# Optimization experiments

Measured on AMD Instinct MI355X. Metric: run time of the kernel, lower is better.

The kernel has to match this reference:

```python
import jax, jax.numpy as jnp
import numpy as np

NUM_HEADS = 4
WINDOW = 3

def setup_inputs() -> dict:
    key = jax.random.key(0)
    ks = jax.random.split(key, 6)
    B, V, C, H, W = 4, 6, 256, 32, 32
    s = 0.02
    return {
        "x": jax.random.normal(ks[0], (B, V, C, H, W), jnp.float32),
        "Wq": jax.random.normal(ks[1], (C, C), jnp.float32) * s,
        "bq": jnp.zeros((C,), jnp.float32),
        "Wk": jax.random.normal(ks[2], (V * C, C), jnp.float32) * s,
        "bk": jnp.zeros((C,), jnp.float32),
        "Wv": jax.random.normal(ks[3], (V * C, C), jnp.float32) * s,
        "bv": jnp.zeros((C,), jnp.float32),
        "Wo": jax.random.normal(ks[4], (C, C), jnp.float32) * s,
        "bo": jnp.zeros((C,), jnp.float32),
    }

def reference(x, Wq, bq, Wk, bk, Wv, bv, Wo, bo):
    B, V, C, H, W = x.shape
    HW = H * W
    S = HW * V  # query sequence length
    nh = NUM_HEADS
    hd = C // nh
    # q: [B, V, H, W, C] -> [B, S, C]
    q_in = jnp.transpose(x, (0, 1, 3, 4, 2)).reshape(B, S, C)
    # k/v input: [B, H, W, V, C] -> [B, HW, V*C]
    kv_in = jnp.transpose(x, (0, 3, 4, 1, 2)).reshape(B, HW, V * C)
    q = q_in @ Wq + bq
    k = kv_in @ Wk + bk
    v = kv_in @ Wv + bv
    q = q.reshape(B, S, nh, hd).transpose(0, 2, 1, 3)    # [B, nh, S, hd]
    k = k.reshape(B, HW, nh, hd).transpose(0, 2, 1, 3)   # [B, nh, HW, hd]
    v = v.reshape(B, HW, nh, hd).transpose(0, 2, 1, 3)   # [B, nh, HW, hd]
    logits = jnp.einsum("bhqd,bhkd->bhqk", q, k) / jnp.sqrt(jnp.float32(hd))
    # Faithful mask: row i has ones in columns [max(0,i-W), i+W] (clipped to HW cols);
    # it is ADDED as mask * -1e9, masking OUT the diagonal window (as in source).
    i = jnp.arange(S)[:, None]
    j = jnp.arange(HW)[None, :]
    mask = ((j >= i - WINDOW) & (j < i + WINDOW + 1)).astype(logits.dtype)
    logits = logits + mask * (-1e9)
    attn = jax.nn.softmax(logits, axis=-1)
    out = jnp.einsum("bhqk,bhkd->bhqd", attn, v)         # [B, nh, S, hd]
    out = out.transpose(0, 2, 1, 3).reshape(B, S, C)
    out = out @ Wo + bo
    return x.reshape(B * V, C, H, W) + out.reshape(B * V, C, H, W)
```

## Files before the change

### kernel.cpp

```cpp
#include <hip/hip_runtime.h>
#include <cstddef>

namespace {

constexpr int B=4, V=6, C=256, HWS=1024, S=6144, NH=4, HD=64, VC=1536;

typedef short short8  __attribute__((ext_vector_type(8)));
typedef short short4v __attribute__((ext_vector_type(4)));
typedef float f32x4   __attribute__((ext_vector_type(4)));

__device__ inline short f2bf(float f){
  union{float f; unsigned u;} v; v.f=f;
  unsigned r = v.u + 0x7fffu + ((v.u>>16)&1u);
  return (short)(r>>16);
}
__device__ inline unsigned fbits(float f){
  union{float f; unsigned u;} v; v.f=f; return v.u;
}

__device__ inline void tr_tile(const float* in, int inRow, short* out, int outRow,
                               int r0, int c0, short* T , int t){
  {
    const int rr=t>>2, cc=(t&3)*16;
    const float* p = in + (size_t)(r0+rr)*inRow + c0 + cc;
    short tmp[16];
    #pragma unroll
    for(int j=0;j<4;j++){
      const float4 f=*(const float4*)(p+j*4);
      tmp[j*4+0]=f2bf(f.x); tmp[j*4+1]=f2bf(f.y);
      tmp[j*4+2]=f2bf(f.z); tmp[j*4+3]=f2bf(f.w);
    }
    *(short8*)&T[rr*72+cc]   = *(short8*)&tmp[0];
    *(short8*)&T[rr*72+cc+8] = *(short8*)&tmp[8];
  }
  __syncthreads();
  {
    const int cc=t>>2, rr0=(t&3)*16;
    short tmp[16];
    #pragma unroll
    for(int j=0;j<16;j++) tmp[j]=T[(rr0+j)*72+cc];
    short* o = out + (size_t)(c0+cc)*outRow + r0 + rr0;
    *(short8*)o     = *(short8*)&tmp[0];
    *(short8*)(o+8) = *(short8*)&tmp[8];
  }
}

__global__ __launch_bounds__(256) void prep(const float* __restrict__ x,
                                            const float* __restrict__ Wq, const float* __restrict__ Wk,
                                            const float* __restrict__ Wv, const float* __restrict__ Wo,
                                            short* __restrict__ xb, short* __restrict__ WqT,
                                            short* __restrict__ WkT, short* __restrict__ WvT,
                                            short* __restrict__ WoT){
  __shared__ short T[64*72];
  const int blk=blockIdx.x;
  if(blk<1536){
    const int bx=blk&15, by=(blk>>4)&3, bv=blk>>6;
    tr_tile(x + (size_t)bv*C*HWS, HWS, xb + (size_t)bv*HWS*C, C, by*64, bx*64, T, threadIdx.x);
  } else {
    const int idx=blk-1536;
    const int tile=idx%96, z=idx/96;
    const float* in; short* out; int R;
    if(z==0){in=Wq; out=WqT; R=C;}
    else if(z==1){in=Wo; out=WoT; R=C;}
    else if(z==2){in=Wk; out=WkT; R=VC;}
    else         {in=Wv; out=WvT; R=VC;}
    const int tilesC=C/64, ntiles=(R/64)*tilesC;
    if(tile>=ntiles) return;
    tr_tile(in, C, out, R, (tile/tilesC)*64, (tile%tilesC)*64, T, threadIdx.x);
  }
}

template<int MODE>
__device__ inline void qo_body(const short* __restrict__ A, const short* __restrict__ BT,
                               const float* __restrict__ bias, const float* __restrict__ xres,
                               void* __restrict__ outv, short* As, short* Bs, int n0, int r0){
  const int t=threadIdx.x, lane=t&63, w=t>>6, quad=lane>>4, ln=lane&15;
  f32x4 acc[2][4];
  #pragma unroll
  for(int rt=0;rt<2;rt++)
    #pragma unroll
    for(int nt=0;nt<4;nt++) acc[rt][nt]=(f32x4)0.f;

  for(int k0=0;k0<C;k0+=64){
    if(k0) __syncthreads();
    { const int r=t>>1, c=(t&1)*32;
      const short* p = A + (size_t)(r0+r)*C + k0 + c;
      #pragma unroll
      for(int j=0;j<4;j++) *(short8*)&As[r*72+c+j*8] = *(const short8*)(p+j*8);
    }
    { const int n=t>>2, c=(t&3)*16;
      const short* p = BT + (size_t)(n0+n)*C + k0 + c;
      *(short8*)&Bs[n*72+c]   = *(const short8*)p;
      *(short8*)&Bs[n*72+c+8] = *(const short8*)(p+8);
    }
    __syncthreads();
    #pragma unroll
    for(int s=0;s<2;s++){
      short8 af0=*(short8*)&As[(w*32+ln)*72    + s*32+quad*8];
      short8 af1=*(short8*)&As[(w*32+16+ln)*72 + s*32+quad*8];
      #pragma unroll
      for(int nt=0;nt<4;nt++){
        const short8 bf=*(short8*)&Bs[(nt*16+ln)*72 + s*32+quad*8];
        acc[0][nt]=__builtin_amdgcn_mfma_f32_16x16x32_bf16(af0,bf,acc[0][nt],0,0,0);
        acc[1][nt]=__builtin_amdgcn_mfma_f32_16x16x32_bf16(af1,bf,acc[1][nt],0,0,0);
      }
    }
  }

  constexpr float QSCALE = 0.18033688011112042f;
  float bcol[4];
  #pragma unroll
  for(int nt=0;nt<4;nt++) bcol[nt]=bias[n0+nt*16+ln];
  #pragma unroll
  for(int rt=0;rt<2;rt++)
    #pragma unroll
    for(int nt=0;nt<4;nt++)
      #pragma unroll
      for(int i=0;i<4;i++){
        const int row=r0+w*32+rt*16+quad*4+i, col=n0+nt*16+ln;
        const float vv=acc[rt][nt][i]+bcol[nt];
        if constexpr(MODE==0) ((short*)outv)[(size_t)row*C+col]=f2bf(vv*QSCALE);
        else ((float*)outv)[(size_t)row*C+col]=vv + xres[(size_t)row*C+col];
      }
}

__global__ __launch_bounds__(256) void proj(const short* __restrict__ xb,
                                            const short* __restrict__ WqT, const short* __restrict__ WkT,
                                            const short* __restrict__ WvT,
                                            const float* __restrict__ bq, const float* __restrict__ bk,
                                            const float* __restrict__ bv,
                                            short* __restrict__ qb, short* __restrict__ Kpack,
                                            short* __restrict__ Vpack){
  __shared__ __align__(16) short sh[13824];
  const int blk=blockIdx.x;
  const int t=threadIdx.x, lane=t&63, w=t>>6, quad=lane>>4, ln=lane&15;

  if(blk>=256){
    const int qblk=blk-256;
    qo_body<0>(xb, WqT, bq, nullptr, qb, sh, sh+9216, (qblk&3)*64, (qblk>>2)*128);
    return;
  }

  short* As=sh; short* Bk=sh+4608; short* Bv=sh+9216;
  const int n0=(blk&3)*64, r0=(blk>>2)*64;
  const int b=r0>>10, hw0=r0&1023;
  const int h=n0>>6, bh=b*NH+h;

  f32x4 ak[4], av[4];
  #pragma unroll
  for(int nt=0;nt<4;nt++){ ak[nt]=(f32x4)0.f; av[nt]=(f32x4)0.f; }

  const int sr=t>>2, sc=(t&3)*16;
  for(int k0=0;k0<VC;k0+=64){
    if(k0) __syncthreads();
    const int v=k0>>8, c0=k0&255;
    { const short* p = xb + (size_t)((b*V+v)*HWS + hw0+sr)*C + c0 + sc;
      *(short8*)&As[sr*72+sc]   = *(const short8*)p;
      *(short8*)&As[sr*72+sc+8] = *(const short8*)(p+8); }
    { const short* p = WkT + (size_t)(n0+sr)*VC + k0 + sc;
      *(short8*)&Bk[sr*72+sc]   = *(const short8*)p;
      *(short8*)&Bk[sr*72+sc+8] = *(const short8*)(p+8); }
    { const short* p = WvT + (size_t)(n0+sr)*VC + k0 + sc;
      *(short8*)&Bv[sr*72+sc]   = *(const short8*)p;
      *(short8*)&Bv[sr*72+sc+8] = *(const short8*)(p+8); }
    __syncthreads();
    #pragma unroll
    for(int s=0;s<2;s++){
      const short8 af=*(short8*)&As[(w*16+ln)*72 + s*32+quad*8];
      #pragma unroll
      for(int nt=0;nt<4;nt++){
        const short8 kf=*(short8*)&Bk[(nt*16+ln)*72 + s*32+quad*8];
        const short8 vf=*(short8*)&Bv[(nt*16+ln)*72 + s*32+quad*8];
        ak[nt]=__builtin_amdgcn_mfma_f32_16x16x32_bf16(af,kf,ak[nt],0,0,0);
        av[nt]=__builtin_amdgcn_mfma_f32_16x16x32_bf16(af,vf,av[nt],0,0,0);
      }
    }
  }

  float bkc[4], bvc[4];
  #pragma unroll
  for(int nt=0;nt<4;nt++){ bkc[nt]=bk[n0+nt*16+ln]; bvc[nt]=bv[n0+nt*16+ln]; }

  {
    short* vq = Vpack + ((size_t)(bh*64 + (hw0>>4) + w))*1024;
    #pragma unroll
    for(int nt=0;nt<4;nt++){
      short4v vp;
      #pragma unroll
      for(int i=0;i<4;i++) vp[i]=f2bf(av[nt][i]+bvc[nt]);
      *(short4v*)(vq + nt*256 + lane*4) = vp;
    }
  }

  __syncthreads();
  #pragma unroll
  for(int nt=0;nt<4;nt++)
    #pragma unroll
    for(int i=0;i<4;i++)
      As[(w*16+quad*4+i)*72 + nt*16+ln] = f2bf(ak[nt][i]+bkc[nt]);
  __syncthreads();
  {
    short* kp = Kpack + ((size_t)(bh*64 + (hw0>>4) + w))*1024;
    #pragma unroll
    for(int half=0; half<2; half++){
      const short8 f = *(short8*)&As[(w*16+ln)*72 + half*32 + quad*8];
      *(short8*)(kp + half*512 + lane*8) = f;
    }
  }
}

__global__ __launch_bounds__(256,4) void attn_k(const short* __restrict__ q, const short* __restrict__ Kpack,
                                                const short* __restrict__ Vpack, short* __restrict__ ao){
  __shared__ float obuf[64*68];
  __shared__ float lbuf[4][32];
  const int blk=blockIdx.x;
  const int bh=(blk&7)*2 + ((blk>>3)&1);
  const int qt=blk>>4;
  const int b=bh>>2, h=bh&3;
  const int s0=qt*64;
  const int t=threadIdx.x, lane=t&63, w=t>>6, quad=lane>>4, ln=lane&15;
  const int wq=w&1, wk=w>>1;

  short8 qf[2][2];
  #pragma unroll
  for(int ntl=0;ntl<2;ntl++)
    #pragma unroll
    for(int s=0;s<2;s++)
      qf[ntl][s]=*(const short8*)&q[(size_t)(b*S+s0+(wq*2+ntl)*16+ln)*C + h*HD + s*32+quad*8];

  f32x4 o[4][2];
  #pragma unroll
  for(int dt=0;dt<4;dt++)
    #pragma unroll
    for(int ntl=0;ntl<2;ntl++) o[dt][ntl]=(f32x4)0.f;
  f32x4 l4[2];
  l4[0]=(f32x4)0.f; l4[1]=(f32x4)0.f;

  const short* kbase = Kpack + ((size_t)bh*64 + wk*2)*1024;
  const short* vbase = Vpack + ((size_t)bh*64 + wk*2)*1024;
  const f32x4 z4=(f32x4)0.f;
  const int rb = s0 + wq*32;

  #pragma unroll 1
  for(int TI=0; TI<16; TI++){
    const short* kp = kbase + (size_t)TI*4096;
    const short* vp = vbase + (size_t)TI*4096;
    const short8 kf00=*(const short8*)(kp + lane*8);
    const short8 kf01=*(const short8*)(kp + 512 + lane*8);
    const short8 kf10=*(const short8*)(kp + 1024 + lane*8);
    const short8 kf11=*(const short8*)(kp + 1536 + lane*8);

    f32x4 sa[2][2];
    #pragma unroll
    for(int ntl=0;ntl<2;ntl++){
      sa[0][ntl]=__builtin_amdgcn_mfma_f32_16x16x32_bf16(kf00,qf[ntl][0],z4,0,0,0);
      sa[0][ntl]=__builtin_amdgcn_mfma_f32_16x16x32_bf16(kf01,qf[ntl][1],sa[0][ntl],0,0,0);
      sa[1][ntl]=__builtin_amdgcn_mfma_f32_16x16x32_bf16(kf10,qf[ntl][0],z4,0,0,0);
      sa[1][ntl]=__builtin_amdgcn_mfma_f32_16x16x32_bf16(kf11,qf[ntl][1],sa[1][ntl],0,0,0);
    }

    short4v vf[2][4];
    #pragma unroll
    for(int kt=0;kt<2;kt++)
      #pragma unroll
      for(int dt=0;dt<4;dt++)
        vf[kt][dt]=*(const short4v*)(vp + kt*1024 + dt*256 + lane*4);

    const int kmin=TI*64 + wk*32;
    if(kmin+31 >= rb-3 && kmin <= rb+34){
      #pragma unroll
      for(int kt=0;kt<2;kt++)
        #pragma unroll
        for(int ntl=0;ntl<2;ntl++){
          const int ig=rb+ntl*16+ln;
          #pragma unroll
          for(int i=0;i<4;i++){
            const int jg=kmin+kt*16+quad*4+i;
            if((unsigned)(jg-ig+3)<=6u) sa[kt][ntl][i]=-100.f;
          }
        }
    }

    short4v pt[2][2];
    #pragma unroll
    for(int kt=0;kt<2;kt++)
      #pragma unroll
      for(int ntl=0;ntl<2;ntl++){
        f32x4 pv;
        #pragma unroll
        for(int i=0;i<4;i++) pv[i]=__builtin_amdgcn_exp2f(sa[kt][ntl][i]);
        l4[ntl]+=pv;
        union{ short4v s; unsigned u[2]; } P;
        P.u[0]=__builtin_amdgcn_perm(fbits(pv[1]), fbits(pv[0]), 0x07060302u);
        P.u[1]=__builtin_amdgcn_perm(fbits(pv[3]), fbits(pv[2]), 0x07060302u);
        pt[kt][ntl]=P.s;
      }

    #pragma unroll
    for(int kt=0;kt<2;kt++)
      #pragma unroll
      for(int dt=0;dt<4;dt++)
        #pragma unroll
        for(int ntl=0;ntl<2;ntl++)
          o[dt][ntl]=__builtin_amdgcn_mfma_f32_16x16x16bf16_1k(vf[kt][dt],pt[kt][ntl],o[dt][ntl],0,0,0);
  }

  float l[2];
  #pragma unroll
  for(int ntl=0;ntl<2;ntl++){
    l[ntl]=l4[ntl][0]+l4[ntl][1]+l4[ntl][2]+l4[ntl][3];
    l[ntl]+=__shfl_xor(l[ntl],16);
    l[ntl]+=__shfl_xor(l[ntl],32);
  }
  if(quad==0){
    lbuf[w][ln]    = l[0];
    lbuf[w][16+ln] = l[1];
  }
  if(wk==0){
    #pragma unroll
    for(int dt=0;dt<4;dt++)
      #pragma unroll
      for(int ntl=0;ntl<2;ntl++)
        #pragma unroll
        for(int i=0;i<4;i++)
          obuf[(dt*16+quad*4+i)*68 + wq*32+ntl*16+ln] = o[dt][ntl][i];
  }
  __syncthreads();
  if(wk==1){
    #pragma unroll
    for(int dt=0;dt<4;dt++)
      #pragma unroll
      for(int ntl=0;ntl<2;ntl++)
        #pragma unroll
        for(int i=0;i<4;i++)
          obuf[(dt*16+quad*4+i)*68 + wq*32+ntl*16+ln] += o[dt][ntl][i];
  }
  __syncthreads();

  {
    const int row=t>>2, dg=t&3;
    const int wqr=row>>5, idx=row&31;
    const float linv=1.0f/(lbuf[wqr][idx]+lbuf[wqr+2][idx]);
    short tmp[16];
    #pragma unroll
    for(int j=0;j<16;j++) tmp[j]=f2bf(obuf[(dg*16+j)*68+row]*linv);
    short* op = ao + (size_t)(b*S+s0+row)*C + h*HD + dg*16;
    *(short8*)op     = *(short8*)&tmp[0];
    *(short8*)(op+8) = *(short8*)&tmp[8];
  }
}

__global__ __launch_bounds__(256) void o_gemm(const short* __restrict__ A, const short* __restrict__ BT,
                                              const float* __restrict__ bias, const float* __restrict__ xres,
                                              float* __restrict__ out){
  __shared__ __align__(16) short sh[13824];
  qo_body<1>(A, BT, bias, xres, out, sh, sh+9216, (int)(blockIdx.x&3)*64, (int)(blockIdx.x>>2)*128);
}

}

extern "C" void kernel_launch(void* const* d_in, const int* in_sizes, int n_in,
                              void* d_out, int out_size, void* d_ws, size_t ws_size,
                              hipStream_t stream) {
  const float* x  = (const float*)d_in[0];
  const float* Wq = (const float*)d_in[1];
  const float* bq = (const float*)d_in[2];
  const float* Wk = (const float*)d_in[3];
  const float* bk = (const float*)d_in[4];
  const float* Wv = (const float*)d_in[5];
  const float* bv = (const float*)d_in[6];
  const float* Wo = (const float*)d_in[7];
  const float* bo = (const float*)d_in[8];
  float* out = (float*)d_out;

  char* p = (char*)d_ws;
  const size_t szBS=(size_t)B*S*C*2, szK=(size_t)B*HWS*C*2;
  short* xb   =(short*)p; p+=szBS;
  short* qb   =(short*)p; p+=szBS;
  short* aob  =(short*)p; p+=szBS;
  short* Kpack=(short*)p; p+=szK;
  short* Vpack=(short*)p; p+=szK;
  short* WqT=(short*)p; p+=(size_t)C*C*2;
  short* WoT=(short*)p; p+=(size_t)C*C*2;
  short* WkT=(short*)p; p+=(size_t)C*VC*2;
  short* WvT=(short*)p; p+=(size_t)C*VC*2;

  prep<<<dim3(1920), 256, 0, stream>>>(x, Wq,Wk,Wv,Wo, xb, WqT,WkT,WvT,WoT);
  proj<<<dim3(1024), 256, 0, stream>>>(xb, WqT,WkT,WvT, bq,bk,bv, qb, Kpack, Vpack);
  attn_k<<<dim3(B*NH*(S/64)), 256, 0, stream>>>(qb, Kpack, Vpack, aob);
  o_gemm<<<dim3(4*((B*S)/128)), 256, 0, stream>>>(aob, WoT, bo, x, out);
}
```

Measured before the change: 190.2 us.

## Stage K/V tiles in LDS with double-buffered async loads; widen attention blocks

The attention kernel now uses 512-thread blocks covering 128 query rows. K/V tiles are loaded with global_load_lds into a double-buffered shared-memory area that is reused for the output reduction, which halves the number of times each K/V tile is fetched from global memory. The prep transpose drops its LDS staging and the barrier: each thread transposes a 4x4 register block and writes strided 8-byte stores. The trade-off is a barrier every iteration and less efficient stores in the transpose.

```diff
diff --git a/kernel.cpp b/kernel.cpp
--- a/kernel.cpp
+++ b/kernel.cpp
@@ -18,30 +18,27 @@
   union{float f; unsigned u;} v; v.f=f; return v.u;
 }
 
+typedef const __attribute__((address_space(1))) unsigned* gas_t;
+typedef __attribute__((address_space(3))) unsigned* las_t;
+__device__ inline void gll(const void* g, void* l){
+  __builtin_amdgcn_global_load_lds((gas_t)g, (las_t)l, 16, 0, 0);
+}
+
 __device__ inline void tr_tile(const float* in, int inRow, short* out, int outRow,
-                               int r0, int c0, short* T , int t){
-  {
-    const int rr=t>>2, cc=(t&3)*16;
-    const float* p = in + (size_t)(r0+rr)*inRow + c0 + cc;
-    short tmp[16];
-    #pragma unroll
-    for(int j=0;j<4;j++){
-      const float4 f=*(const float4*)(p+j*4);
-      tmp[j*4+0]=f2bf(f.x); tmp[j*4+1]=f2bf(f.y);
-      tmp[j*4+2]=f2bf(f.z); tmp[j*4+3]=f2bf(f.w);
-    }
-    *(short8*)&T[rr*72+cc]   = *(short8*)&tmp[0];
-    *(short8*)&T[rr*72+cc+8] = *(short8*)&tmp[8];
-  }
-  __syncthreads();
-  {
-    const int cc=t>>2, rr0=(t&3)*16;
-    short tmp[16];
-    #pragma unroll
-    for(int j=0;j<16;j++) tmp[j]=T[(rr0+j)*72+cc];
-    short* o = out + (size_t)(c0+cc)*outRow + r0 + rr0;
-    *(short8*)o     = *(short8*)&tmp[0];
-    *(short8*)(o+8) = *(short8*)&tmp[8];
+                               int r0, int c0, int t){
+  const int tx=t&15, ty=t>>4;
+  float a[4][4];
+  #pragma unroll
+  for(int i=0;i<4;i++){
+    const float4 f=*(const float4*)(in + (size_t)(r0+ty*4+i)*inRow + c0 + tx*4);
+    a[i][0]=f.x; a[i][1]=f.y; a[i][2]=f.z; a[i][3]=f.w;
+  }
+  #pragma unroll
+  for(int j=0;j<4;j++){
+    short4v o4;
+    #pragma unroll
+    for(int i=0;i<4;i++) o4[i]=f2bf(a[i][j]);
+    *(short4v*)(out + (size_t)(c0+tx*4+j)*outRow + r0+ty*4) = o4;
   }
 }
 
@@ -51,11 +48,10 @@
                                             short* __restrict__ xb, short* __restrict__ WqT,
                                             short* __restrict__ WkT, short* __restrict__ WvT,
                                             short* __restrict__ WoT){
-  __shared__ short T[64*72];
   const int blk=blockIdx.x;
   if(blk<1536){
     const int bx=blk&15, by=(blk>>4)&3, bv=blk>>6;
-    tr_tile(x + (size_t)bv*C*HWS, HWS, xb + (size_t)bv*HWS*C, C, by*64, bx*64, T, threadIdx.x);
+    tr_tile(x + (size_t)bv*C*HWS, HWS, xb + (size_t)bv*HWS*C, C, by*64, bx*64, threadIdx.x);
   } else {
     const int idx=blk-1536;
     const int tile=idx%96, z=idx/96;
@@ -66,7 +62,7 @@
     else         {in=Wv; out=WvT; R=VC;}
     const int tilesC=C/64, ntiles=(R/64)*tilesC;
     if(tile>=ntiles) return;
-    tr_tile(in, C, out, R, (tile/tilesC)*64, (tile%tilesC)*64, T, threadIdx.x);
+    tr_tile(in, C, out, R, (tile/tilesC)*64, (tile%tilesC)*64, threadIdx.x);
   }
 }
 
@@ -209,24 +205,27 @@
   }
 }
 
-__global__ __launch_bounds__(256,4) void attn_k(const short* __restrict__ q, const short* __restrict__ Kpack,
+__global__ __launch_bounds__(512,4) void attn_k(const short* __restrict__ q, const short* __restrict__ Kpack,
                                                 const short* __restrict__ Vpack, short* __restrict__ ao){
-  __shared__ float obuf[64*68];
-  __shared__ float lbuf[4][32];
+  __shared__ __align__(16) char smem[34816];
+  short* KV   = (short*)smem;
+  float* obuf = (float*)smem;
+  float* lbuf = (float*)(smem + 33792);
+
   const int blk=blockIdx.x;
   const int bh=(blk&7)*2 + ((blk>>3)&1);
   const int qt=blk>>4;
   const int b=bh>>2, h=bh&3;
-  const int s0=qt*64;
+  const int s0=qt*128;
   const int t=threadIdx.x, lane=t&63, w=t>>6, quad=lane>>4, ln=lane&15;
-  const int wq=w&1, wk=w>>1;
+  const int wq=w&3, wk=w>>2;
 
   short8 qf[2][2];
   #pragma unroll
   for(int ntl=0;ntl<2;ntl++)
     #pragma unroll
     for(int s=0;s<2;s++)
-      qf[ntl][s]=*(const short8*)&q[(size_t)(b*S+s0+(wq*2+ntl)*16+ln)*C + h*HD + s*32+quad*8];
+      qf[ntl][s]=*(const short8*)&q[(size_t)(b*S+s0+wq*32+ntl*16+ln)*C + h*HD + s*32+quad*8];
 
   f32x4 o[4][2];
   #pragma unroll
@@ -236,19 +235,29 @@
   f32x4 l4[2];
   l4[0]=(f32x4)0.f; l4[1]=(f32x4)0.f;
 
-  const short* kbase = Kpack + ((size_t)bh*64 + wk*2)*1024;
-  const short* vbase = Vpack + ((size_t)bh*64 + wk*2)*1024;
+  const short* Kt = Kpack + (size_t)bh*65536;
+  const short* Vt = Vpack + (size_t)bh*65536;
   const f32x4 z4=(f32x4)0.f;
   const int rb = s0 + wq*32;
 
+  gll(Kt + w*512 + lane*8, KV + w*512);
+  gll(Vt + 0*4096 + w*512 + lane*8, KV + 4096 + w*512);
+  __syncthreads();
+
   #pragma unroll 1
   for(int TI=0; TI<16; TI++){
-    const short* kp = kbase + (size_t)TI*4096;
-    const short* vp = vbase + (size_t)TI*4096;
-    const short8 kf00=*(const short8*)(kp + lane*8);
-    const short8 kf01=*(const short8*)(kp + 512 + lane*8);
-    const short8 kf10=*(const short8*)(kp + 1024 + lane*8);
-    const short8 kf11=*(const short8*)(kp + 1536 + lane*8);
+    if(TI<15){
+      const int nb=(TI+1)&1;
+      gll(Kt + (size_t)(TI+1)*4096 + w*512 + lane*8, KV + nb*8192 + w*512);
+      gll(Vt + (size_t)(TI+1)*4096 + w*512 + lane*8, KV + nb*8192 + 4096 + w*512);
+    }
+    const short* Kb = KV + (TI&1)*8192;
+    const short* Vb = Kb + 4096;
+
+    const short8 kf00=*(const short8*)&Kb[wk*2048 + lane*8];
+    const short8 kf01=*(const short8*)&Kb[wk*2048 + 512 + lane*8];
+    const short8 kf10=*(const short8*)&Kb[wk*2048 + 1024 + lane*8];
+    const short8 kf11=*(const short8*)&Kb[wk*2048 + 1536 + lane*8];
 
     f32x4 sa[2][2];
     #pragma unroll
@@ -264,7 +273,7 @@
     for(int kt=0;kt<2;kt++)
       #pragma unroll
       for(int dt=0;dt<4;dt++)
-        vf[kt][dt]=*(const short4v*)(vp + kt*1024 + dt*256 + lane*4);
+        vf[kt][dt]=*(const short4v*)&Vb[wk*2048 + kt*1024 + dt*256 + lane*4];
 
     const int kmin=TI*64 + wk*32;
     if(kmin+31 >= rb-3 && kmin <= rb+34){
@@ -303,6 +312,8 @@
         #pragma unroll
         for(int ntl=0;ntl<2;ntl++)
           o[dt][ntl]=__builtin_amdgcn_mfma_f32_16x16x16bf16_1k(vf[kt][dt],pt[kt][ntl],o[dt][ntl],0,0,0);
+
+    __syncthreads();
   }
 
   float l[2];
@@ -313,8 +324,8 @@
     l[ntl]+=__shfl_xor(l[ntl],32);
   }
   if(quad==0){
-    lbuf[w][ln]    = l[0];
-    lbuf[w][16+ln] = l[1];
+    lbuf[w*32+ln]    = l[0];
+    lbuf[w*32+16+ln] = l[1];
   }
   if(wk==0){
     #pragma unroll
@@ -323,7 +334,7 @@
       for(int ntl=0;ntl<2;ntl++)
         #pragma unroll
         for(int i=0;i<4;i++)
-          obuf[(dt*16+quad*4+i)*68 + wq*32+ntl*16+ln] = o[dt][ntl][i];
+          obuf[(dt*16+quad*4+i)*132 + wq*32+ntl*16+ln] = o[dt][ntl][i];
   }
   __syncthreads();
   if(wk==1){
@@ -333,17 +344,16 @@
       for(int ntl=0;ntl<2;ntl++)
         #pragma unroll
         for(int i=0;i<4;i++)
-          obuf[(dt*16+quad*4+i)*68 + wq*32+ntl*16+ln] += o[dt][ntl][i];
+          obuf[(dt*16+quad*4+i)*132 + wq*32+ntl*16+ln] += o[dt][ntl][i];
   }
   __syncthreads();
 
   {
     const int row=t>>2, dg=t&3;
-    const int wqr=row>>5, idx=row&31;
-    const float linv=1.0f/(lbuf[wqr][idx]+lbuf[wqr+2][idx]);
+    const float linv=1.0f/(lbuf[(row>>5)*32 + (row&31)] + lbuf[(4+(row>>5))*32 + (row&31)]);
     short tmp[16];
     #pragma unroll
-    for(int j=0;j<16;j++) tmp[j]=f2bf(obuf[(dg*16+j)*68+row]*linv);
+    for(int j=0;j<16;j++) tmp[j]=f2bf(obuf[(dg*16+j)*132+row]*linv);
     short* op = ao + (size_t)(b*S+s0+row)*C + h*HD + dg*16;
     *(short8*)op     = *(short8*)&tmp[0];
     *(short8*)(op+8) = *(short8*)&tmp[8];
@@ -387,6 +397,6 @@
 
   prep<<<dim3(1920), 256, 0, stream>>>(x, Wq,Wk,Wv,Wo, xb, WqT,WkT,WvT,WoT);
   proj<<<dim3(1024), 256, 0, stream>>>(xb, WqT,WkT,WvT, bq,bk,bv, qb, Kpack, Vpack);
-  attn_k<<<dim3(B*NH*(S/64)), 256, 0, stream>>>(qb, Kpack, Vpack, aob);
+  attn_k<<<dim3(B*NH*(S/128)), 512, 0, stream>>>(qb, Kpack, Vpack, aob);
   o_gemm<<<dim3(4*((B*S)/128)), 256, 0, stream>>>(aob, WoT, bo, x, out);
 }
```

Result: faster. 184.3 us (-3.1%).
